# Optimization experiments

Hardware: AMD Instinct MI355X
Metric: run time of the kernel (lower is better)

The kernel has to match this reference:

```python
import jax, jax.numpy as jnp
import numpy as np

D_MODEL = 2048
N_EXPERTS = 64
TOP_K = 2
AUX_LOSS_COEF = 0.01
ENTROPY_COEF = 0.01


def setup_inputs() -> dict:
    key = jax.random.key(0)
    kx, kw = jax.random.split(key)
    x = jax.random.normal(kx, (4, 4096, D_MODEL), dtype=jnp.float32)
    # nn.Linear(d_model, n_experts, bias=False) weight: [E, D]
    W = jax.random.normal(kw, (N_EXPERTS, D_MODEL), dtype=jnp.float32) * 0.02
    temp = jnp.ones((1,), dtype=jnp.float32)
    return {"x": x, "W": W, "temp": temp}


def reference(x, W, temp):
    B, S, D = x.shape
    E = W.shape[0]
    # gate logits: [B,S,E]
    logits = jnp.einsum("bsd,ed->bse", x, W)
    t = jnp.clip(temp, 0.1, 5.0)  # self.temp.clamp(0.1, 5.0); eval mode -> no noise
    probs = jax.nn.softmax(logits / t, axis=-1)
    expert_probs, expert_indices = jax.lax.top_k(probs, TOP_K)  # [B,S,K]
    # scatter ones at top-k indices -> [B,S,E]
    expert_mask = jax.nn.one_hot(expert_indices, E, dtype=probs.dtype).sum(axis=-2)
    # aux losses
    importance = probs.mean(axis=(0, 1))                 # [E]
    load = expert_mask.sum(axis=(0, 1)) / (B * S + 1e-6)  # [E]
    aux_load_loss = (importance * load).sum() * E * AUX_LOSS_COEF
    token_entropy = -(probs * jnp.log(jnp.clip(probs, 1e-8))).sum(axis=-1).mean()
    router_entropy = token_entropy * ENTROPY_COEF
    return (expert_probs, expert_indices, expert_mask, aux_load_loss, router_entropy)
```

## Files before the change

### kernel.cpp

```cpp
#include <hip/hip_runtime.h>
#include <hip/hip_bf16.h>
#include <math.h>

#define D_MODEL 2048
#define N_EXP   64
#define NTOK    16384
#define NBLK    512
#define NSTG    16

typedef short bf16x8 __attribute__((ext_vector_type(8)));
typedef float f32x16 __attribute__((ext_vector_type(16)));
typedef unsigned int u32;

#define OFF_PROBS 0
#define OFF_IDX   32768
#define OFF_MASK  65536
#define OFF_AUX   1114112
#define OFF_ENT   1114113

#define WF_PS 16384

__device__ __forceinline__ void split3(float xv, u32& h, u32& m, u32& l) {
  u32 xb = __builtin_bit_cast(u32, xv);
  u32 hb = xb & 0xFFFF0000u;
  float tf = xv - __builtin_bit_cast(float, hb);
  u32 tb = __builtin_bit_cast(u32, tf);
  u32 mb = tb & 0xFFFF0000u;
  float t2 = tf - __builtin_bit_cast(float, mb);
  u32 lb = __builtin_bit_cast(u32, t2);
  h = hb >> 16; m = mb >> 16; l = lb >> 16;
}

__device__ __forceinline__ bool better(float a, int ia, float b, int ib) {
  return (a > b) || (a == b && ia < ib);
}

__global__ __launch_bounds__(256) void wprep_kernel(
    const float* __restrict__ W, bf16x8* __restrict__ Wf) {
  int gid  = blockIdx.x * 256 + threadIdx.x;
  int g    = gid >> 7;
  int n    = (gid >> 6) & 1;
  int lane = gid & 63;
  int e    = n * 32 + (lane & 31);
  int k    = g * 16 + ((lane >> 5) << 3);
  const float* wr = W + (size_t)e * D_MODEL + k;
  bf16x8 hv, mv, lv;
#pragma unroll
  for (int j = 0; j < 8; ++j) {
    u32 h, m, l;
    split3(wr[j], h, m, l);
    hv[j] = (short)h; mv[j] = (short)m; lv[j] = (short)l;
  }
  Wf[gid]             = hv;
  Wf[WF_PS + gid]     = mv;
  Wf[2 * WF_PS + gid] = lv;
}

__global__ __launch_bounds__(512, 4) void fused_kernel(
    const float* __restrict__ x, const bf16x8* __restrict__ Wf,
    const float* __restrict__ temp, float* __restrict__ out,
    float* __restrict__ imp_part, float* __restrict__ load_part,
    float* __restrict__ ent_part) {
  __shared__ float lds[16384];
  const int tid  = threadIdx.x;
  const int w    = tid >> 6;
  const int lane = tid & 63;
  const int t0   = blockIdx.x * 32;
  const int rl   = lane & 31;
  const int hg   = lane >> 5;

  float tv = temp[0];
  tv = fminf(fmaxf(tv, 0.1f), 5.0f);
  const float invT = 1.0f / tv;

  const float* gsrc[2];
#pragma unroll
  for (int i = 0; i < 2; ++i) {
    int tl = i * 16 + (lane >> 2);
    gsrc[i] = x + (size_t)(t0 + tl) * D_MODEL + w * 16
            + (((lane & 3) ^ (tl & 3)) << 2);
  }
  float* const wbase = lds + w * 2048;

  auto stageW = [&](int s) {
    float* dst = wbase + (s & 3) * 512;
#pragma unroll
    for (int i = 0; i < 2; ++i) {
      __builtin_amdgcn_global_load_lds(
          (const __attribute__((address_space(1))) void*)(gsrc[i] + s * 128),
          (__attribute__((address_space(3))) void*)(dst + i * 256),
          16, 0, 0);
    }
  };
  auto loadB = [&](int st, bf16x8* bb) {
    const bf16x8* wp = Wf + (size_t)(st * 8 + w) * 128 + lane;
#pragma unroll
    for (int p = 0; p < 3; ++p)
#pragma unroll
      for (int n = 0; n < 2; ++n)
        bb[p * 2 + n] = wp[p * WF_PS + n * 64];
  };

  f32x16 acc0, acc1;
#pragma unroll
  for (int i = 0; i < 16; ++i) { acc0[i] = 0.0f; acc1[i] = 0.0f; }

  bf16x8 b[2][6];
  stageW(0); stageW(1); stageW(2);
  loadB(0, b[0]);

#pragma unroll
  for (int st = 0; st < NSTG; ++st) {
    if (st + 3 < NSTG) stageW(st + 3);
    if (st + 1 < NSTG) loadB(st + 1, b[(st + 1) & 1]);

    if (st <= 12)      asm volatile("s_waitcnt vmcnt(18)" ::: "memory");
    else if (st == 13) asm volatile("s_waitcnt vmcnt(16)" ::: "memory");
    else if (st == 14) asm volatile("s_waitcnt vmcnt(14)" ::: "memory");
    else               asm volatile("s_waitcnt vmcnt(6)"  ::: "memory");
    __builtin_amdgcn_sched_barrier(0);

    const float* rb = wbase + (st & 3) * 512 + rl * 16;
    float4 a0 = *(const float4*)(rb + (((hg * 2)     ^ (rl & 3)) << 2));
    float4 a1 = *(const float4*)(rb + (((hg * 2 + 1) ^ (rl & 3)) << 2));
    float av[8] = {a0.x, a0.y, a0.z, a0.w, a1.x, a1.y, a1.z, a1.w};
    bf16x8 ah, am, al;
#pragma unroll
    for (int j = 0; j < 8; ++j) {
      u32 hh, mm, ll;
      split3(av[j], hh, mm, ll);
      ah[j] = (short)hh; am[j] = (short)mm; al[j] = (short)ll;
    }
    const bf16x8* bb = b[st & 1];
    acc0 = __builtin_amdgcn_mfma_f32_32x32x16_bf16(ah, bb[0], acc0, 0, 0, 0);
    acc1 = __builtin_amdgcn_mfma_f32_32x32x16_bf16(ah, bb[1], acc1, 0, 0, 0);
    acc0 = __builtin_amdgcn_mfma_f32_32x32x16_bf16(ah, bb[2], acc0, 0, 0, 0);
    acc1 = __builtin_amdgcn_mfma_f32_32x32x16_bf16(ah, bb[3], acc1, 0, 0, 0);
    acc0 = __builtin_amdgcn_mfma_f32_32x32x16_bf16(am, bb[0], acc0, 0, 0, 0);
    acc1 = __builtin_amdgcn_mfma_f32_32x32x16_bf16(am, bb[1], acc1, 0, 0, 0);
    acc0 = __builtin_amdgcn_mfma_f32_32x32x16_bf16(am, bb[2], acc0, 0, 0, 0);
    acc1 = __builtin_amdgcn_mfma_f32_32x32x16_bf16(am, bb[3], acc1, 0, 0, 0);
    acc0 = __builtin_amdgcn_mfma_f32_32x32x16_bf16(ah, bb[4], acc0, 0, 0, 0);
    acc1 = __builtin_amdgcn_mfma_f32_32x32x16_bf16(ah, bb[5], acc1, 0, 0, 0);
    acc0 = __builtin_amdgcn_mfma_f32_32x32x16_bf16(al, bb[0], acc0, 0, 0, 0);
    acc1 = __builtin_amdgcn_mfma_f32_32x32x16_bf16(al, bb[1], acc1, 0, 0, 0);
  }

  __syncthreads();
#pragma unroll
  for (int r = 0; r < 16; ++r) {
    int row = (r & 3) + ((r >> 2) << 3) + (hg << 2);
    lds[w * 2048 + row * 64 + rl]      = acc0[r];
    lds[w * 2048 + row * 64 + 32 + rl] = acc1[r];
  }
  __syncthreads();

  const int row  = tid >> 4;
  const int colq = tid & 15;
  float l0 = 0.f, l1 = 0.f, l2 = 0.f, l3 = 0.f;
  for (int wv = 0; wv < 8; ++wv) {
    float4 v = *(const float4*)&lds[wv * 2048 + row * 64 + colq * 4];
    l0 += v.x; l1 += v.y; l2 += v.z; l3 += v.w;
  }
  l0 *= invT; l1 *= invT; l2 *= invT; l3 *= invT;

  float m = fmaxf(fmaxf(l0, l1), fmaxf(l2, l3));
#pragma unroll
  for (int d = 1; d < 16; d <<= 1) m = fmaxf(m, __shfl_xor(m, d));

  float ls0 = l0 - m, ls1 = l1 - m, ls2 = l2 - m, ls3 = l3 - m;
  float e0 = __expf(ls0), e1 = __expf(ls1), e2 = __expf(ls2), e3 = __expf(ls3);
  float ssum = e0 + e1 + e2 + e3;
  float dot  = e0 * ls0 + e1 * ls1 + e2 * ls2 + e3 * ls3;
#pragma unroll
  for (int d = 1; d < 16; d <<= 1) {
    ssum += __shfl_xor(ssum, d);
    dot  += __shfl_xor(dot, d);
  }
  const float inv_s = 1.0f / ssum;
  const float ent = __logf(ssum) - dot * inv_s;

  const int eb = colq * 4;
  float b1 = e0, b2 = -1.0f;
  int   i1 = eb, i2 = eb + 1;
  {
    float ev[3] = {e1, e2, e3};
#pragma unroll
    for (int j = 0; j < 3; ++j) {
      int ej = eb + 1 + j;
      if (better(ev[j], ej, b1, i1)) { b2 = b1; i2 = i1; b1 = ev[j]; i1 = ej; }
      else if (better(ev[j], ej, b2, i2)) { b2 = ev[j]; i2 = ej; }
    }
  }
#pragma unroll
  for (int d = 1; d < 16; d <<= 1) {
    float ob1 = __shfl_xor(b1, d), ob2 = __shfl_xor(b2, d);
    int   oi1 = __shfl_xor(i1, d), oi2 = __shfl_xor(i2, d);
    if (better(ob1, oi1, b1, i1)) {
      if (better(b1, i1, ob2, oi2)) { b2 = b1; i2 = i1; }
      else                          { b2 = ob2; i2 = oi2; }
      b1 = ob1; i1 = oi1;
    } else if (better(ob1, oi1, b2, i2)) {
      b2 = ob1; i2 = oi1;
    }
  }

  const int t = t0 + row;
  if (colq == 0) {
    out[OFF_PROBS + (size_t)t * 2 + 0] = b1 * inv_s;
    out[OFF_PROBS + (size_t)t * 2 + 1] = b2 * inv_s;
    out[OFF_IDX   + (size_t)t * 2 + 0] = (float)i1;
    out[OFF_IDX   + (size_t)t * 2 + 1] = (float)i2;
  }
  {
    float4 mv;
    mv.x = ((eb + 0 == i1) || (eb + 0 == i2)) ? 1.0f : 0.0f;
    mv.y = ((eb + 1 == i1) || (eb + 1 == i2)) ? 1.0f : 0.0f;
    mv.z = ((eb + 2 == i1) || (eb + 2 == i2)) ? 1.0f : 0.0f;
    mv.w = ((eb + 3 == i1) || (eb + 3 == i2)) ? 1.0f : 0.0f;
    *(float4*)&out[OFF_MASK + (size_t)t * N_EXP + eb] = mv;
  }

  __syncthreads();
  {
    float4 p4;
    p4.x = e0 * inv_s; p4.y = e1 * inv_s; p4.z = e2 * inv_s; p4.w = e3 * inv_s;
    *(float4*)&lds[row * 64 + eb] = p4;
  }
  if (colq == 0) {
    lds[2048 + row] = (float)i1;
    lds[2080 + row] = (float)i2;
    lds[2112 + row] = ent;
  }
  __syncthreads();
  if (tid < 64) {
    float simp = 0.0f, sld = 0.0f;
    const float fe = (float)tid;
    for (int r = 0; r < 32; ++r) simp += lds[r * 64 + tid];
    for (int r = 0; r < 32; ++r)
      sld += ((lds[2048 + r] == fe) ? 1.0f : 0.0f)
           + ((lds[2080 + r] == fe) ? 1.0f : 0.0f);
    imp_part[blockIdx.x * N_EXP + tid]  = simp;
    load_part[blockIdx.x * N_EXP + tid] = sld;
    float v = (tid < 32) ? lds[2112 + tid] : 0.0f;
#pragma unroll
    for (int d = 1; d < 64; d <<= 1) v += __shfl_xor(v, d);
    if (tid == 0) ent_part[blockIdx.x] = v;
  }
}

__global__ __launch_bounds__(256) void finalize_part(
    const float* __restrict__ imp_part, const float* __restrict__ load_part,
    const float* __restrict__ ent_part, float* __restrict__ imp2,
    float* __restrict__ load2, float* __restrict__ ent2) {
  __shared__ float si[4][64], sl[4][64], se[4];
  const int tid  = threadIdx.x;
  const int lane = tid & 63;
  const int q    = tid >> 6;
  const int base = blockIdx.x * 8 + q * 2;
  float a = imp_part[(size_t)base * N_EXP + lane]
          + imp_part[(size_t)(base + 1) * N_EXP + lane];
  float b = load_part[(size_t)base * N_EXP + lane]
          + load_part[(size_t)(base + 1) * N_EXP + lane];
  si[q][lane] = a;
  sl[q][lane] = b;
  if (lane == 0) se[q] = ent_part[base] + ent_part[base + 1];
  __syncthreads();
  if (tid < 64) {
    imp2[blockIdx.x * N_EXP + tid]  = si[0][tid] + si[1][tid] + si[2][tid] + si[3][tid];
    load2[blockIdx.x * N_EXP + tid] = sl[0][tid] + sl[1][tid] + sl[2][tid] + sl[3][tid];
    if (tid == 0) ent2[blockIdx.x] = se[0] + se[1] + se[2] + se[3];
  }
}

__global__ __launch_bounds__(256) void finalize_final(
    const float* __restrict__ imp2, const float* __restrict__ load2,
    const float* __restrict__ ent2, float* __restrict__ out) {
  __shared__ float si[4][64], sl[4][64];
  const int tid  = threadIdx.x;
  const int lane = tid & 63;
  const int q    = tid >> 6;
  float a = 0.0f, b = 0.0f;
  for (int r = q * 16; r < q * 16 + 16; ++r) {
    a += imp2[r * N_EXP + lane];
    b += load2[r * N_EXP + lane];
  }
  si[q][lane] = a;
  sl[q][lane] = b;
  __syncthreads();
  if (tid < 64) {
    float imp = si[0][tid] + si[1][tid] + si[2][tid] + si[3][tid];
    float ld  = sl[0][tid] + sl[1][tid] + sl[2][tid] + sl[3][tid];
    imp *= (1.0f / 16384.0f);
    ld  *= (1.0f / (16384.0f + 1e-6f));
    float prod = imp * ld;
    float e = ent2[tid];
#pragma unroll
    for (int d = 1; d < 64; d <<= 1) {
      prod += __shfl_xor(prod, d);
      e    += __shfl_xor(e, d);
    }
    if (tid == 0) {
      out[OFF_AUX] = prod * 64.0f * 0.01f;
      out[OFF_ENT] = (e / 16384.0f) * 0.01f;
    }
  }
}

extern "C" void kernel_launch(void* const* d_in, const int* in_sizes, int n_in,
                              void* d_out, int out_size, void* d_ws, size_t ws_size,
                              hipStream_t stream) {
  const float* x    = (const float*)d_in[0];
  const float* W    = (const float*)d_in[1];
  const float* temp = (const float*)d_in[2];
  float* out = (float*)d_out;
  float* ws  = (float*)d_ws;

  bf16x8* Wf    = (bf16x8*)ws;
  float*  imp   = ws + 196608;
  float*  ldp   = imp + NBLK * N_EXP;
  float*  entp  = ldp + NBLK * N_EXP;
  float*  imp2  = entp + NBLK;
  float*  load2 = imp2 + 64 * N_EXP;
  float*  ent2  = load2 + 64 * N_EXP;

  wprep_kernel<<<64, 256, 0, stream>>>(W, Wf);
  fused_kernel<<<NBLK, 512, 0, stream>>>(x, Wf, temp, out, imp, ldp, entp);
  finalize_part<<<64, 256, 0, stream>>>(imp, ldp, entp, imp2, load2, ent2);
  finalize_final<<<1, 256, 0, stream>>>(imp2, load2, ent2, out);
}
```

Before: 53.39 us.

## Load x directly into registers instead of staging through LDS

Replaces the async global_load_lds staging of x tiles (3-deep LDS ring with manual vmcnt waits) with direct float4 global loads into a two-stage register double buffer, prefetched two steps ahead alongside the W fragments. This removes the LDS round trip, the swizzled LDS reads and the hand-tuned waitcnt sequence. In exchange it raises register pressure, leaves wait placement to the compiler, and each lane's loads are strided across token rows, so coalescing may be worse than the staged path.

```diff
diff --git a/kernel.cpp b/kernel.cpp
--- a/kernel.cpp
+++ b/kernel.cpp
@@ -73,25 +73,8 @@
   tv = fminf(fmaxf(tv, 0.1f), 5.0f);
   const float invT = 1.0f / tv;
 
-  const float* gsrc[2];
-#pragma unroll
-  for (int i = 0; i < 2; ++i) {
-    int tl = i * 16 + (lane >> 2);
-    gsrc[i] = x + (size_t)(t0 + tl) * D_MODEL + w * 16
-            + (((lane & 3) ^ (tl & 3)) << 2);
-  }
-  float* const wbase = lds + w * 2048;
-
-  auto stageW = [&](int s) {
-    float* dst = wbase + (s & 3) * 512;
-#pragma unroll
-    for (int i = 0; i < 2; ++i) {
-      __builtin_amdgcn_global_load_lds(
-          (const __attribute__((address_space(1))) void*)(gsrc[i] + s * 128),
-          (__attribute__((address_space(3))) void*)(dst + i * 256),
-          16, 0, 0);
-    }
-  };
+  const float* ax = x + (size_t)(t0 + rl) * D_MODEL + w * 16 + hg * 8;
+
   auto loadB = [&](int st, bf16x8* bb) {
     const bf16x8* wp = Wf + (size_t)(st * 8 + w) * 128 + lane;
 #pragma unroll
@@ -105,24 +88,28 @@
 #pragma unroll
   for (int i = 0; i < 16; ++i) { acc0[i] = 0.0f; acc1[i] = 0.0f; }
 
+  float4 a[2][2];
   bf16x8 b[2][6];
-  stageW(0); stageW(1); stageW(2);
+
+  a[0][0] = *(const float4*)(ax + 0);
+  a[0][1] = *(const float4*)(ax + 4);
+  a[1][0] = *(const float4*)(ax + 128);
+  a[1][1] = *(const float4*)(ax + 132);
   loadB(0, b[0]);
+  loadB(1, b[1]);
 
 #pragma unroll
   for (int st = 0; st < NSTG; ++st) {
-    if (st + 3 < NSTG) stageW(st + 3);
-    if (st + 1 < NSTG) loadB(st + 1, b[(st + 1) & 1]);
-
-    if (st <= 12)      asm volatile("s_waitcnt vmcnt(18)" ::: "memory");
-    else if (st == 13) asm volatile("s_waitcnt vmcnt(16)" ::: "memory");
-    else if (st == 14) asm volatile("s_waitcnt vmcnt(14)" ::: "memory");
-    else               asm volatile("s_waitcnt vmcnt(6)"  ::: "memory");
-    __builtin_amdgcn_sched_barrier(0);
-
-    const float* rb = wbase + (st & 3) * 512 + rl * 16;
-    float4 a0 = *(const float4*)(rb + (((hg * 2)     ^ (rl & 3)) << 2));
-    float4 a1 = *(const float4*)(rb + (((hg * 2 + 1) ^ (rl & 3)) << 2));
+    float4 a0 = a[st & 1][0];
+    float4 a1 = a[st & 1][1];
+    bf16x8 bb0 = b[st & 1][0], bb1 = b[st & 1][1], bb2 = b[st & 1][2];
+    bf16x8 bb3 = b[st & 1][3], bb4 = b[st & 1][4], bb5 = b[st & 1][5];
+    if (st + 2 < NSTG) {
+      a[st & 1][0] = *(const float4*)(ax + (st + 2) * 128);
+      a[st & 1][1] = *(const float4*)(ax + (st + 2) * 128 + 4);
+      loadB(st + 2, b[st & 1]);
+    }
+
     float av[8] = {a0.x, a0.y, a0.z, a0.w, a1.x, a1.y, a1.z, a1.w};
     bf16x8 ah, am, al;
 #pragma unroll
@@ -131,19 +118,18 @@
       split3(av[j], hh, mm, ll);
       ah[j] = (short)hh; am[j] = (short)mm; al[j] = (short)ll;
     }
-    const bf16x8* bb = b[st & 1];
-    acc0 = __builtin_amdgcn_mfma_f32_32x32x16_bf16(ah, bb[0], acc0, 0, 0, 0);
-    acc1 = __builtin_amdgcn_mfma_f32_32x32x16_bf16(ah, bb[1], acc1, 0, 0, 0);
-    acc0 = __builtin_amdgcn_mfma_f32_32x32x16_bf16(ah, bb[2], acc0, 0, 0, 0);
-    acc1 = __builtin_amdgcn_mfma_f32_32x32x16_bf16(ah, bb[3], acc1, 0, 0, 0);
-    acc0 = __builtin_amdgcn_mfma_f32_32x32x16_bf16(am, bb[0], acc0, 0, 0, 0);
-    acc1 = __builtin_amdgcn_mfma_f32_32x32x16_bf16(am, bb[1], acc1, 0, 0, 0);
-    acc0 = __builtin_amdgcn_mfma_f32_32x32x16_bf16(am, bb[2], acc0, 0, 0, 0);
-    acc1 = __builtin_amdgcn_mfma_f32_32x32x16_bf16(am, bb[3], acc1, 0, 0, 0);
-    acc0 = __builtin_amdgcn_mfma_f32_32x32x16_bf16(ah, bb[4], acc0, 0, 0, 0);
-    acc1 = __builtin_amdgcn_mfma_f32_32x32x16_bf16(ah, bb[5], acc1, 0, 0, 0);
-    acc0 = __builtin_amdgcn_mfma_f32_32x32x16_bf16(al, bb[0], acc0, 0, 0, 0);
-    acc1 = __builtin_amdgcn_mfma_f32_32x32x16_bf16(al, bb[1], acc1, 0, 0, 0);
+    acc0 = __builtin_amdgcn_mfma_f32_32x32x16_bf16(ah, bb0, acc0, 0, 0, 0);
+    acc1 = __builtin_amdgcn_mfma_f32_32x32x16_bf16(ah, bb1, acc1, 0, 0, 0);
+    acc0 = __builtin_amdgcn_mfma_f32_32x32x16_bf16(ah, bb2, acc0, 0, 0, 0);
+    acc1 = __builtin_amdgcn_mfma_f32_32x32x16_bf16(ah, bb3, acc1, 0, 0, 0);
+    acc0 = __builtin_amdgcn_mfma_f32_32x32x16_bf16(am, bb0, acc0, 0, 0, 0);
+    acc1 = __builtin_amdgcn_mfma_f32_32x32x16_bf16(am, bb1, acc1, 0, 0, 0);
+    acc0 = __builtin_amdgcn_mfma_f32_32x32x16_bf16(am, bb2, acc0, 0, 0, 0);
+    acc1 = __builtin_amdgcn_mfma_f32_32x32x16_bf16(am, bb3, acc1, 0, 0, 0);
+    acc0 = __builtin_amdgcn_mfma_f32_32x32x16_bf16(ah, bb4, acc0, 0, 0, 0);
+    acc1 = __builtin_amdgcn_mfma_f32_32x32x16_bf16(ah, bb5, acc1, 0, 0, 0);
+    acc0 = __builtin_amdgcn_mfma_f32_32x32x16_bf16(al, bb0, acc0, 0, 0, 0);
+    acc1 = __builtin_amdgcn_mfma_f32_32x32x16_bf16(al, bb1, acc1, 0, 0, 0);
   }
 
   __syncthreads();
```

New measurement: 54.96 us. 2.9% more time.
